# Kernel tuning notes

Hardware: AMD Instinct MI355X
Metric: run time of the kernel (lower is better)

Reference implementation:

```python
import jax, jax.numpy as jnp
import numpy as np

DIST = 3.0
COEFF = 10.0
NEG_SLOPE = 0.3  # keras LeakyReLU default


def _probe_points(dist=DIST):
    # fixed 26 probe offsets on a sphere of radius `dist` (from build())
    angles = np.array(
        [[j * 0.125 - 0.125, i * 0.125 + (j - 1) * 0.0625] for j in range(3) for i in range(8)]
        + [[-0.25, 0.0], [0.25, 0.0]],
        dtype=np.float32,
    ) * (2.0 * np.pi)
    a, b = angles[:, 0], angles[:, 1]
    pts = np.stack([np.sin(a), np.cos(a) * np.cos(b), np.cos(a) * np.sin(b)], axis=-1) * dist
    return jnp.asarray(pts, dtype=jnp.float32)  # (26, 3)


def setup_inputs() -> dict:
    key = jax.random.key(0)
    k1, k2, k3 = jax.random.split(key, 3)
    B, n, f = 2, 1024, 3
    m, out_feats, num_convs = 26, 6, 5
    points = jax.random.normal(k1, (B, n, 3 + f), dtype=jnp.float32)
    # per-conv Dense(m*f -> out_feats) weights/bias, stacked over num_convs
    W = jax.random.normal(k2, (num_convs, m * f, out_feats), dtype=jnp.float32) * 0.1
    b = jax.random.normal(k3, (num_convs, out_feats), dtype=jnp.float32) * 0.1
    return {"points": points, "W": W, "b": b}


def reference(points, W, b):
    B, n, df = points.shape
    d = 3
    f = df - d
    probes = _probe_points()              # (m, d)
    m = probes.shape[0]
    coords = points[..., :d]              # (B, n, d) -> centers too (l = n)
    feats = points[..., d:]               # (B, n, f)
    centers = coords
    # probes per center: (B, l, m, d)
    probes_per_center = centers[:, :, None, :] + probes[None, None, :, :]
    # delta: (B, l, m, n, d)
    delta = coords[:, None, None, :, :] - probes_per_center[:, :, :, None, :]
    sq = jnp.sum(delta * delta, axis=-1)  # (B, l, m, n)
    wgt = COEFF / (sq + COEFF)            # inverse-distance weights
    # weighted feature sum: (B, l, m, f), averaged over n
    wf = jnp.einsum('blmn,bnf->blmf', wgt, feats) / n
    x = wf.reshape(B, n, m * f)           # (B, l, m*f)
    # num_convs parallel Dense + LeakyReLU (Dropout is identity at inference)
    h = jnp.einsum('blx,kxo->blko', x, W) + b[None, None, :, :]
    h = jnp.where(h > 0, h, NEG_SLOPE * h)
    convs = h.reshape(B, n, -1)           # (B, n, num_convs*out_feats)
    return jnp.concatenate([centers, convs], axis=-1)  # (B, n, 3 + 30)
```

## Files before the change

kernel.cpp:

```cpp
#include <hip/hip_runtime.h>


#define NPTS   1024
#define COEFF  10.0f
#define NEG    0.3f

typedef float  v2f __attribute__((ext_vector_type(2)));
typedef __fp16 h2  __attribute__((ext_vector_type(2)));

#define CA 4.24264068f
#define CY 3.91968890f
#define CZ 1.62358830f

constexpr int M0[14] = {0,5, 1,4, 2,3, 7,6, 8,12, 10,14, 24,25};
constexpr int M1[12] = {16,19, 17,18, 20,23, 21,22, 9,13, 11,15};

__device__ __forceinline__ v2f pk_fma(v2f a, v2f b, v2f c) {
  v2f d;
  asm("v_pk_fma_f32 %0, %1, %2, %3" : "=v"(d) : "v"(a), "v"(b), "v"(c));
  return d;
}
__device__ __forceinline__ v2f pk_fma_n(v2f a, v2f b, v2f c) {
  v2f d;
  asm("v_pk_fma_f32 %0, %1, %2, %3 neg_lo:[1,0,0] neg_hi:[1,0,0]"
      : "=v"(d) : "v"(a), "v"(b), "v"(c));
  return d;
}
__device__ __forceinline__ v2f pk_add(v2f a, v2f b) {
  v2f d;
  asm("v_pk_add_f32 %0, %1, %2" : "=v"(d) : "v"(a), "v"(b));
  return d;
}
__device__ __forceinline__ v2f pk_sub(v2f a, v2f b) {
  v2f d;
  asm("v_pk_add_f32 %0, %1, %2 neg_lo:[0,1] neg_hi:[0,1]"
      : "=v"(d) : "v"(a), "v"(b));
  return d;
}

#define DPP_H2(x, ctrl, rm, bm, bc)                                          \
  x = x + __builtin_bit_cast(h2, __builtin_amdgcn_update_dpp(                \
      0, __builtin_bit_cast(int, x), ctrl, rm, bm, bc))

__device__ __forceinline__ h2 h2_wave_sum_to_lane63(h2 x) {
  DPP_H2(x, 0x111, 0xf, 0xf, true);
  DPP_H2(x, 0x112, 0xf, 0xf, true);
  DPP_H2(x, 0x114, 0xf, 0xe, false);
  DPP_H2(x, 0x118, 0xf, 0xc, false);
  DPP_H2(x, 0x142, 0xa, 0xf, false);
  DPP_H2(x, 0x143, 0xc, 0xf, false);
  return x;
}

__device__ __forceinline__ void rcp8_cvt(const v2f* t, h2* wp) {
  const float p0 = t[0].x * t[0].y, p1 = t[1].x * t[1].y;
  const float p2 = t[2].x * t[2].y, p3 = t[3].x * t[3].y;
  const float q01 = p0 * p1, q23 = p2 * p3;
  const float r   = __builtin_amdgcn_rcpf(q01 * q23);
  const float r01 = q23 * r, r23 = q01 * r;
  const float i0 = p1 * r01, i1 = p0 * r01;
  const float i2 = p3 * r23, i3 = p2 * r23;
  wp[0] = __builtin_amdgcn_cvt_pkrtz(t[0].y * i0, t[0].x * i0);
  wp[1] = __builtin_amdgcn_cvt_pkrtz(t[1].y * i1, t[1].x * i1);
  wp[2] = __builtin_amdgcn_cvt_pkrtz(t[2].y * i2, t[2].x * i2);
  wp[3] = __builtin_amdgcn_cvt_pkrtz(t[3].y * i3, t[3].x * i3);
}
__device__ __forceinline__ void rcp4_cvt(const v2f* t, h2* wp) {
  const float p0 = t[0].x * t[0].y, p1 = t[1].x * t[1].y;
  const float r  = __builtin_amdgcn_rcpf(p0 * p1);
  const float i0 = p1 * r, i1 = p0 * r;
  wp[0] = __builtin_amdgcn_cvt_pkrtz(t[0].y * i0, t[0].x * i0);
  wp[1] = __builtin_amdgcn_cvt_pkrtz(t[1].y * i1, t[1].x * i1);
}

template <int HALF>
__device__ void run_main(const float* __restrict__ sxyz,
                         const h2* __restrict__ sfeat,
                         int lane, v2f cxp, v2f cyp, v2f czp, float* acc) {
  constexpr int NP = HALF ? 12 : 14;
  const v2f kCA = {CA, CA}, kCY = {CY, CY}, kCZ = {CZ, CZ};
  const v2f k6 = {6.f, 6.f}, k19 = {19.f, 19.f};

  v2f px[2], py[2], pz[2];
  h2  f0[2], f1[2], f2[2];

#define LOADIT(buf, it)                                                       \
  {                                                                           \
    const int nb = (it) * 128 + 2 * lane;                                     \
    const int nh = (it) * 64 + lane;                                          \
    px[buf] = *reinterpret_cast<const v2f*>(&sxyz[0 * NPTS + nb]);            \
    py[buf] = *reinterpret_cast<const v2f*>(&sxyz[1 * NPTS + nb]);            \
    pz[buf] = *reinterpret_cast<const v2f*>(&sxyz[2 * NPTS + nb]);            \
    f0[buf] = sfeat[0 * (NPTS / 2) + nh];                                     \
    f1[buf] = sfeat[1 * (NPTS / 2) + nh];                                     \
    f2[buf] = sfeat[2 * (NPTS / 2) + nh];                                     \
  }

  LOADIT(0, 0);
  #pragma unroll
  for (int it = 0; it < 8; ++it) {
    const int cur = it & 1, nxt = cur ^ 1;
    if (it < 7) LOADIT(nxt, it + 1);

    const v2f dx = pk_sub(px[cur], cxp);
    const v2f dy = pk_sub(py[cur], cyp);
    const v2f dz = pk_sub(pz[cur], czp);
    v2f base = pk_fma(dz, dz, k19);
    base = pk_fma(dy, dy, base);
    base = pk_fma(dx, dx, base);

    v2f t[NP];
    if constexpr (HALF == 0) {
      const v2f rx = pk_fma(kCA, dx, base);
      const v2f sA = pk_fma  (kCZ, dz, rx);
      const v2f sB = pk_fma_n(kCZ, dz, rx);
      const v2f sC = pk_fma_n(kCY, dz, rx);
      const v2f sD = pk_fma  (kCY, dz, rx);
      t[0]  = pk_fma_n(kCY, dy, sA);  t[1]  = pk_fma(kCY, dy, sA);
      t[2]  = pk_fma_n(kCY, dy, sB);  t[3]  = pk_fma(kCY, dy, sB);
      t[4]  = pk_fma_n(kCZ, dy, sC);  t[5]  = pk_fma(kCZ, dy, sC);
      t[6]  = pk_fma_n(kCZ, dy, sD);  t[7]  = pk_fma(kCZ, dy, sD);
      t[8]  = pk_fma_n(k6, dy, base); t[9]  = pk_fma(k6, dy, base);
      t[10] = pk_fma_n(k6, dz, base); t[11] = pk_fma(k6, dz, base);
      t[12] = pk_fma  (k6, dx, base); t[13] = pk_fma_n(k6, dx, base);
    } else {
      const v2f rx = pk_fma_n(kCA, dx, base);
      const v2f sA = pk_fma_n(kCZ, dz, rx);
      const v2f sB = pk_fma_n(kCY, dz, rx);
      const v2f sC = pk_fma  (kCZ, dz, rx);
      const v2f sD = pk_fma  (kCY, dz, rx);
      const v2f u = pk_add(dy, dz), v = pk_sub(dy, dz);
      t[0]  = pk_fma_n(kCY, dy, sA);  t[1]  = pk_fma(kCY, dy, sA);
      t[2]  = pk_fma_n(kCZ, dy, sB);  t[3]  = pk_fma(kCZ, dy, sB);
      t[4]  = pk_fma  (kCY, dy, sC);  t[5]  = pk_fma_n(kCY, dy, sC);
      t[6]  = pk_fma  (kCZ, dy, sD);  t[7]  = pk_fma_n(kCZ, dy, sD);
      t[8]  = pk_fma_n(kCA, u, base); t[9]  = pk_fma(kCA, u, base);
      t[10] = pk_fma  (kCA, v, base); t[11] = pk_fma_n(kCA, v, base);
    }

    h2 wp[NP];
    rcp8_cvt(t + 0, wp + 0);
    rcp8_cvt(t + 4, wp + 4);
    rcp8_cvt(t + 8, wp + 8);
    if constexpr (NP == 14) rcp4_cvt(t + 12, wp + 12);

    #pragma unroll
    for (int j = 0; j < NP; ++j) {
      acc[j * 3 + 0] = __builtin_amdgcn_fdot2(wp[j], f0[cur], acc[j * 3 + 0], false);
      acc[j * 3 + 1] = __builtin_amdgcn_fdot2(wp[j], f1[cur], acc[j * 3 + 1], false);
      acc[j * 3 + 2] = __builtin_amdgcn_fdot2(wp[j], f2[cur], acc[j * 3 + 2], false);
    }
  }
#undef LOADIT
}

template <int HALF>
__device__ __forceinline__ void reduce_store(float* acc, int lane, float* sx) {
  constexpr int NP = HALF ? 12 : 14;
  constexpr int NH = NP * 3 / 2;
  h2 red[NH];
  #pragma unroll
  for (int p = 0; p < NH; ++p)
    red[p] = __builtin_amdgcn_cvt_pkrtz(acc[2 * p], acc[2 * p + 1]);
  #pragma unroll
  for (int p = 0; p < NH; ++p)
    red[p] = h2_wave_sum_to_lane63(red[p]);
  if (lane == 63) {
    #pragma unroll
    for (int p = 0; p < NH; ++p) {
      const int a0 = 2 * p, a1 = 2 * p + 1;
      const int m0 = (HALF ? M1[a0 / 3] : M0[a0 / 3]);
      const int m1 = (HALF ? M1[a1 / 3] : M0[a1 / 3]);
      sx[m0 * 3 + a0 % 3] = (float)red[p].x;
      sx[m1 * 3 + a1 % 3] = (float)red[p].y;
    }
  }
}

__global__ __launch_bounds__(256, 4) void crossconv_kernel(
    const float* __restrict__ points,
    const float* __restrict__ W,
    const float* __restrict__ bias,
    float* __restrict__ out)
{
    __shared__ __align__(16) float sxyz[3 * NPTS];
    __shared__ __align__(16) h2    sfeat[3 * NPTS / 2];
    __shared__ __align__(16) float sx[2][80];

    const int tid    = threadIdx.x;
    const int lane   = tid & 63;
    const int w      = tid >> 6;
    const int cLocal = w >> 1;
    const int half   = w & 1;
    const int G      = blockIdx.x * 2 + cLocal;

    const float* batch = points + (G >> 10) * (NPTS * 6);

    {
      const float4* src4 = reinterpret_cast<const float4*>(batch) + 6 * tid;
      const float4 q0 = src4[0], q1 = src4[1], q2 = src4[2];
      const float4 q3 = src4[3], q4 = src4[4], q5 = src4[5];
      const int r = 4 * tid;
      sxyz[0*NPTS + r+0] = q0.x; sxyz[1*NPTS + r+0] = q0.y; sxyz[2*NPTS + r+0] = q0.z;
      sxyz[0*NPTS + r+1] = q1.z; sxyz[1*NPTS + r+1] = q1.w; sxyz[2*NPTS + r+1] = q2.x;
      sxyz[0*NPTS + r+2] = q3.x; sxyz[1*NPTS + r+2] = q3.y; sxyz[2*NPTS + r+2] = q3.z;
      sxyz[0*NPTS + r+3] = q4.z; sxyz[1*NPTS + r+3] = q4.w; sxyz[2*NPTS + r+3] = q5.x;
      const int h = r >> 1;
      sfeat[0*(NPTS/2) + h+0] = __builtin_amdgcn_cvt_pkrtz(q0.w, q2.y);
      sfeat[0*(NPTS/2) + h+1] = __builtin_amdgcn_cvt_pkrtz(q3.w, q5.y);
      sfeat[1*(NPTS/2) + h+0] = __builtin_amdgcn_cvt_pkrtz(q1.x, q2.z);
      sfeat[1*(NPTS/2) + h+1] = __builtin_amdgcn_cvt_pkrtz(q4.x, q5.z);
      sfeat[2*(NPTS/2) + h+0] = __builtin_amdgcn_cvt_pkrtz(q1.y, q2.w);
      sfeat[2*(NPTS/2) + h+1] = __builtin_amdgcn_cvt_pkrtz(q4.y, q5.w);
    }
    __syncthreads();

    const int   ci = ((blockIdx.x & 511) << 1) | cLocal;
    const float cx = sxyz[0*NPTS + ci], cy = sxyz[1*NPTS + ci], cz = sxyz[2*NPTS + ci];
    const v2f cxp = {cx, cx}, cyp = {cy, cy}, czp = {cz, cz};

    float acc[42];
    #pragma unroll
    for (int j = 0; j < 42; ++j) acc[j] = 0.f;

    if (half == 0) run_main<0>(sxyz, sfeat, lane, cxp, cyp, czp, acc);
    else           run_main<1>(sxyz, sfeat, lane, cxp, cyp, czp, acc);

    if (half == 0) reduce_store<0>(acc, lane, sx[cLocal]);
    else           reduce_store<1>(acc, lane, sx[cLocal]);
    __syncthreads();

    if (half == 0) {
      const float scale = COEFF / (float)NPTS;
      float* orow = out + G * 33;
      if (lane < 30) {
        const int k = lane / 6, o = lane % 6;
        const float* Wk = W + k * (78 * 6) + o;
        float h0 = 0.f, h1 = 0.f, h2_ = 0.f, h3 = 0.f;
        const float4* sxv = reinterpret_cast<const float4*>(sx[cLocal]);
        #pragma unroll
        for (int t4 = 0; t4 < 19; ++t4) {
          const float4 v = sxv[t4];
          h0  = fmaf(v.x, Wk[(t4 * 4 + 0) * 6], h0);
          h1  = fmaf(v.y, Wk[(t4 * 4 + 1) * 6], h1);
          h2_ = fmaf(v.z, Wk[(t4 * 4 + 2) * 6], h2_);
          h3  = fmaf(v.w, Wk[(t4 * 4 + 3) * 6], h3);
        }
        const float2 vt = *reinterpret_cast<const float2*>(&sx[cLocal][76]);
        h0 = fmaf(vt.x, Wk[76 * 6], h0);
        h1 = fmaf(vt.y, Wk[77 * 6], h1);
        const float dot = (h0 + h2_) + (h1 + h3);
        float h = fmaf(dot, scale, bias[lane]);
        h = (h > 0.f) ? h : NEG * h;
        orow[3 + lane] = h;
      } else if (lane < 33) {
        orow[lane - 30] = (lane == 30) ? cx : ((lane == 31) ? cy : cz);
      }
    }
}

extern "C" void kernel_launch(void* const* d_in, const int* in_sizes, int n_in,
                              void* d_out, int out_size, void* d_ws, size_t ws_size,
                              hipStream_t stream) {
    const float* points = (const float*)d_in[0];
    const float* W      = (const float*)d_in[1];
    const float* bias   = (const float*)d_in[2];
    float* out          = (float*)d_out;
    crossconv_kernel<<<1024, 256, 0, stream>>>(points, W, bias, out);
}
```

Baseline: 21.27 us.

## Split neighbor loop across two waves per probe half with 512-thread blocks

Doubles the block to 512 threads so each (center, probe-half) pair gets two waves, each processing half of the 1024 neighbor points. Partial sums from both waves are written to separate shared slots and added in the final dense layer. The point staging is spread across twice as many threads. This shortens each wave's serial loop and raises parallelism, at the cost of an extra wave reduction, more shared memory and fewer resident blocks per CU.

Result: slower. 24.93 us (+17.2%).

```diff
diff --git a/kernel.cpp b/kernel.cpp
--- a/kernel.cpp
+++ b/kernel.cpp
@@ -76,7 +76,8 @@
 template <int HALF>
 __device__ void run_main(const float* __restrict__ sxyz,
                          const h2* __restrict__ sfeat,
-                         int lane, v2f cxp, v2f cyp, v2f czp, float* acc) {
+                         int nnH, int lane,
+                         v2f cxp, v2f cyp, v2f czp, float* acc) {
   constexpr int NP = HALF ? 12 : 14;
   const v2f kCA = {CA, CA}, kCY = {CY, CY}, kCZ = {CZ, CZ};
   const v2f k6 = {6.f, 6.f}, k19 = {19.f, 19.f};
@@ -86,8 +87,8 @@
 
 #define LOADIT(buf, it)                                                       \
   {                                                                           \
-    const int nb = (it) * 128 + 2 * lane;                                     \
-    const int nh = (it) * 64 + lane;                                          \
+    const int nb = nnH * 512 + (it) * 128 + 2 * lane;                         \
+    const int nh = nnH * 256 + (it) * 64 + lane;                              \
     px[buf] = *reinterpret_cast<const v2f*>(&sxyz[0 * NPTS + nb]);            \
     py[buf] = *reinterpret_cast<const v2f*>(&sxyz[1 * NPTS + nb]);            \
     pz[buf] = *reinterpret_cast<const v2f*>(&sxyz[2 * NPTS + nb]);            \
@@ -98,9 +99,9 @@
 
   LOADIT(0, 0);
   #pragma unroll
-  for (int it = 0; it < 8; ++it) {
+  for (int it = 0; it < 4; ++it) {
     const int cur = it & 1, nxt = cur ^ 1;
-    if (it < 7) LOADIT(nxt, it + 1);
+    if (it < 3) LOADIT(nxt, it + 1);
 
     const v2f dx = pk_sub(px[cur], cxp);
     const v2f dy = pk_sub(py[cur], cyp);
@@ -177,7 +178,7 @@
   }
 }
 
-__global__ __launch_bounds__(256, 4) void crossconv_kernel(
+__global__ __launch_bounds__(512, 4) void crossconv_kernel(
     const float* __restrict__ points,
     const float* __restrict__ W,
     const float* __restrict__ bias,
@@ -185,33 +186,27 @@
 {
     __shared__ __align__(16) float sxyz[3 * NPTS];
     __shared__ __align__(16) h2    sfeat[3 * NPTS / 2];
-    __shared__ __align__(16) float sx[2][80];
+    __shared__ __align__(16) float sx[2][2][80];
 
     const int tid    = threadIdx.x;
     const int lane   = tid & 63;
     const int w      = tid >> 6;
-    const int cLocal = w >> 1;
-    const int half   = w & 1;
+    const int cLocal = w >> 2;
+    const int half   = (w >> 1) & 1;
+    const int nnH    = w & 1;
     const int G      = blockIdx.x * 2 + cLocal;
 
     const float* batch = points + (G >> 10) * (NPTS * 6);
 
     {
-      const float4* src4 = reinterpret_cast<const float4*>(batch) + 6 * tid;
+      const float4* src4 = reinterpret_cast<const float4*>(batch) + 3 * tid;
       const float4 q0 = src4[0], q1 = src4[1], q2 = src4[2];
-      const float4 q3 = src4[3], q4 = src4[4], q5 = src4[5];
-      const int r = 4 * tid;
+      const int r = 2 * tid;
       sxyz[0*NPTS + r+0] = q0.x; sxyz[1*NPTS + r+0] = q0.y; sxyz[2*NPTS + r+0] = q0.z;
       sxyz[0*NPTS + r+1] = q1.z; sxyz[1*NPTS + r+1] = q1.w; sxyz[2*NPTS + r+1] = q2.x;
-      sxyz[0*NPTS + r+2] = q3.x; sxyz[1*NPTS + r+2] = q3.y; sxyz[2*NPTS + r+2] = q3.z;
-      sxyz[0*NPTS + r+3] = q4.z; sxyz[1*NPTS + r+3] = q4.w; sxyz[2*NPTS + r+3] = q5.x;
-      const int h = r >> 1;
-      sfeat[0*(NPTS/2) + h+0] = __builtin_amdgcn_cvt_pkrtz(q0.w, q2.y);
-      sfeat[0*(NPTS/2) + h+1] = __builtin_amdgcn_cvt_pkrtz(q3.w, q5.y);
-      sfeat[1*(NPTS/2) + h+0] = __builtin_amdgcn_cvt_pkrtz(q1.x, q2.z);
-      sfeat[1*(NPTS/2) + h+1] = __builtin_amdgcn_cvt_pkrtz(q4.x, q5.z);
-      sfeat[2*(NPTS/2) + h+0] = __builtin_amdgcn_cvt_pkrtz(q1.y, q2.w);
-      sfeat[2*(NPTS/2) + h+1] = __builtin_amdgcn_cvt_pkrtz(q4.y, q5.w);
+      sfeat[0*(NPTS/2) + tid] = __builtin_amdgcn_cvt_pkrtz(q0.w, q2.y);
+      sfeat[1*(NPTS/2) + tid] = __builtin_amdgcn_cvt_pkrtz(q1.x, q2.z);
+      sfeat[2*(NPTS/2) + tid] = __builtin_amdgcn_cvt_pkrtz(q1.y, q2.w);
     }
     __syncthreads();
 
@@ -223,32 +218,32 @@
     #pragma unroll
     for (int j = 0; j < 42; ++j) acc[j] = 0.f;
 
-    if (half == 0) run_main<0>(sxyz, sfeat, lane, cxp, cyp, czp, acc);
-    else           run_main<1>(sxyz, sfeat, lane, cxp, cyp, czp, acc);
-
-    if (half == 0) reduce_store<0>(acc, lane, sx[cLocal]);
-    else           reduce_store<1>(acc, lane, sx[cLocal]);
+    if (half == 0) run_main<0>(sxyz, sfeat, nnH, lane, cxp, cyp, czp, acc);
+    else           run_main<1>(sxyz, sfeat, nnH, lane, cxp, cyp, czp, acc);
+
+    if (half == 0) reduce_store<0>(acc, lane, sx[cLocal][nnH]);
+    else           reduce_store<1>(acc, lane, sx[cLocal][nnH]);
     __syncthreads();
 
-    if (half == 0) {
+    if ((w & 3) == 0) {
       const float scale = COEFF / (float)NPTS;
       float* orow = out + G * 33;
       if (lane < 30) {
         const int k = lane / 6, o = lane % 6;
         const float* Wk = W + k * (78 * 6) + o;
         float h0 = 0.f, h1 = 0.f, h2_ = 0.f, h3 = 0.f;
-        const float4* sxv = reinterpret_cast<const float4*>(sx[cLocal]);
+        const float4* s0 = reinterpret_cast<const float4*>(sx[cLocal][0]);
+        const float4* s1 = reinterpret_cast<const float4*>(sx[cLocal][1]);
         #pragma unroll
         for (int t4 = 0; t4 < 19; ++t4) {
-          const float4 v = sxv[t4];
-          h0  = fmaf(v.x, Wk[(t4 * 4 + 0) * 6], h0);
-          h1  = fmaf(v.y, Wk[(t4 * 4 + 1) * 6], h1);
-          h2_ = fmaf(v.z, Wk[(t4 * 4 + 2) * 6], h2_);
-          h3  = fmaf(v.w, Wk[(t4 * 4 + 3) * 6], h3);
+          const float4 va = s0[t4], vb = s1[t4];
+          h0  = fmaf(va.x + vb.x, Wk[(t4 * 4 + 0) * 6], h0);
+          h1  = fmaf(va.y + vb.y, Wk[(t4 * 4 + 1) * 6], h1);
+          h2_ = fmaf(va.z + vb.z, Wk[(t4 * 4 + 2) * 6], h2_);
+          h3  = fmaf(va.w + vb.w, Wk[(t4 * 4 + 3) * 6], h3);
         }
-        const float2 vt = *reinterpret_cast<const float2*>(&sx[cLocal][76]);
-        h0 = fmaf(vt.x, Wk[76 * 6], h0);
-        h1 = fmaf(vt.y, Wk[77 * 6], h1);
+        h0 = fmaf(sx[cLocal][0][76] + sx[cLocal][1][76], Wk[76 * 6], h0);
+        h1 = fmaf(sx[cLocal][0][77] + sx[cLocal][1][77], Wk[77 * 6], h1);
         const float dot = (h0 + h2_) + (h1 + h3);
         float h = fmaf(dot, scale, bias[lane]);
         h = (h > 0.f) ? h : NEG * h;
@@ -266,5 +261,5 @@
     const float* W      = (const float*)d_in[1];
     const float* bias   = (const float*)d_in[2];
     float* out          = (float*)d_out;
-    crossconv_kernel<<<1024, 256, 0, stream>>>(points, W, bias, out);
-}
+    crossconv_kernel<<<1024, 512, 0, stream>>>(points, W, bias, out);
+}
```

## Double block size to four centers per block and split reciprocals into pairs

Applied to the files above, without the earlier changes.

Launches 512 blocks of 512 threads so each block handles four centers instead of two. This halves how many times the per-batch point cloud is staged into shared memory, and each thread now loads half as much data. Separately, the 8-way shared-reciprocal trick is replaced by 2-way rcp4 groups, which uses more reciprocal instructions but has shorter dependency chains and less register pressure. With launch_bounds(512,4) the compiler may be pushed to fewer registers, which risks spilling the 42 accumulators.

After: 23.17 us. 8.9% more time.

```diff
diff --git a/kernel.cpp b/kernel.cpp
--- a/kernel.cpp
+++ b/kernel.cpp
@@ -52,19 +52,6 @@
   return x;
 }
 
-__device__ __forceinline__ void rcp8_cvt(const v2f* t, h2* wp) {
-  const float p0 = t[0].x * t[0].y, p1 = t[1].x * t[1].y;
-  const float p2 = t[2].x * t[2].y, p3 = t[3].x * t[3].y;
-  const float q01 = p0 * p1, q23 = p2 * p3;
-  const float r   = __builtin_amdgcn_rcpf(q01 * q23);
-  const float r01 = q23 * r, r23 = q01 * r;
-  const float i0 = p1 * r01, i1 = p0 * r01;
-  const float i2 = p3 * r23, i3 = p2 * r23;
-  wp[0] = __builtin_amdgcn_cvt_pkrtz(t[0].y * i0, t[0].x * i0);
-  wp[1] = __builtin_amdgcn_cvt_pkrtz(t[1].y * i1, t[1].x * i1);
-  wp[2] = __builtin_amdgcn_cvt_pkrtz(t[2].y * i2, t[2].x * i2);
-  wp[3] = __builtin_amdgcn_cvt_pkrtz(t[3].y * i3, t[3].x * i3);
-}
 __device__ __forceinline__ void rcp4_cvt(const v2f* t, h2* wp) {
   const float p0 = t[0].x * t[0].y, p1 = t[1].x * t[1].y;
   const float r  = __builtin_amdgcn_rcpf(p0 * p1);
@@ -139,9 +126,12 @@
     }
 
     h2 wp[NP];
-    rcp8_cvt(t + 0, wp + 0);
-    rcp8_cvt(t + 4, wp + 4);
-    rcp8_cvt(t + 8, wp + 8);
+    rcp4_cvt(t + 0,  wp + 0);
+    rcp4_cvt(t + 2,  wp + 2);
+    rcp4_cvt(t + 4,  wp + 4);
+    rcp4_cvt(t + 6,  wp + 6);
+    rcp4_cvt(t + 8,  wp + 8);
+    rcp4_cvt(t + 10, wp + 10);
     if constexpr (NP == 14) rcp4_cvt(t + 12, wp + 12);
 
     #pragma unroll
@@ -177,7 +167,7 @@
   }
 }
 
-__global__ __launch_bounds__(256, 4) void crossconv_kernel(
+__global__ __launch_bounds__(512, 4) void crossconv_kernel(
     const float* __restrict__ points,
     const float* __restrict__ W,
     const float* __restrict__ bias,
@@ -185,37 +175,30 @@
 {
     __shared__ __align__(16) float sxyz[3 * NPTS];
     __shared__ __align__(16) h2    sfeat[3 * NPTS / 2];
-    __shared__ __align__(16) float sx[2][80];
+    __shared__ __align__(16) float sx[4][80];
 
     const int tid    = threadIdx.x;
     const int lane   = tid & 63;
     const int w      = tid >> 6;
     const int cLocal = w >> 1;
     const int half   = w & 1;
-    const int G      = blockIdx.x * 2 + cLocal;
+    const int G      = blockIdx.x * 4 + cLocal;
 
     const float* batch = points + (G >> 10) * (NPTS * 6);
 
     {
-      const float4* src4 = reinterpret_cast<const float4*>(batch) + 6 * tid;
+      const float4* src4 = reinterpret_cast<const float4*>(batch) + 3 * tid;
       const float4 q0 = src4[0], q1 = src4[1], q2 = src4[2];
-      const float4 q3 = src4[3], q4 = src4[4], q5 = src4[5];
-      const int r = 4 * tid;
+      const int r = 2 * tid;
       sxyz[0*NPTS + r+0] = q0.x; sxyz[1*NPTS + r+0] = q0.y; sxyz[2*NPTS + r+0] = q0.z;
       sxyz[0*NPTS + r+1] = q1.z; sxyz[1*NPTS + r+1] = q1.w; sxyz[2*NPTS + r+1] = q2.x;
-      sxyz[0*NPTS + r+2] = q3.x; sxyz[1*NPTS + r+2] = q3.y; sxyz[2*NPTS + r+2] = q3.z;
-      sxyz[0*NPTS + r+3] = q4.z; sxyz[1*NPTS + r+3] = q4.w; sxyz[2*NPTS + r+3] = q5.x;
-      const int h = r >> 1;
-      sfeat[0*(NPTS/2) + h+0] = __builtin_amdgcn_cvt_pkrtz(q0.w, q2.y);
-      sfeat[0*(NPTS/2) + h+1] = __builtin_amdgcn_cvt_pkrtz(q3.w, q5.y);
-      sfeat[1*(NPTS/2) + h+0] = __builtin_amdgcn_cvt_pkrtz(q1.x, q2.z);
-      sfeat[1*(NPTS/2) + h+1] = __builtin_amdgcn_cvt_pkrtz(q4.x, q5.z);
-      sfeat[2*(NPTS/2) + h+0] = __builtin_amdgcn_cvt_pkrtz(q1.y, q2.w);
-      sfeat[2*(NPTS/2) + h+1] = __builtin_amdgcn_cvt_pkrtz(q4.y, q5.w);
+      sfeat[0*(NPTS/2) + tid] = __builtin_amdgcn_cvt_pkrtz(q0.w, q2.y);
+      sfeat[1*(NPTS/2) + tid] = __builtin_amdgcn_cvt_pkrtz(q1.x, q2.z);
+      sfeat[2*(NPTS/2) + tid] = __builtin_amdgcn_cvt_pkrtz(q1.y, q2.w);
     }
     __syncthreads();
 
-    const int   ci = ((blockIdx.x & 511) << 1) | cLocal;
+    const int   ci = ((blockIdx.x & 255) << 2) | cLocal;
     const float cx = sxyz[0*NPTS + ci], cy = sxyz[1*NPTS + ci], cz = sxyz[2*NPTS + ci];
     const v2f cxp = {cx, cx}, cyp = {cy, cy}, czp = {cz, cz};
 
@@ -266,5 +249,5 @@
     const float* W      = (const float*)d_in[1];
     const float* bias   = (const float*)d_in[2];
     float* out          = (float*)d_out;
-    crossconv_kernel<<<1024, 256, 0, stream>>>(points, W, bias, out);
-}
+    crossconv_kernel<<<512, 512, 0, stream>>>(points, W, bias, out);
+}
```
